# Optimization experiments

Hardware: AMD Instinct MI355X
Metric: run time of the kernel (lower is better)

Reference implementation:

```python
import jax, jax.numpy as jnp
import numpy as np

T, B = 128, 256      # seq_len, batch
D = 1024             # input_dim (embedding dim)
H = 1024             # hidden_dim
NQ = 8               # n_qubits
V = 32000            # vocab_size
TAGS = 1024          # tagset_size


def setup_inputs() -> dict:
    key = jax.random.key(0)
    ks = jax.random.split(key, 10)
    s = 0.05
    return {
        "sentence": jax.random.randint(ks[0], (T, B), 0, V),
        "emb": jax.random.normal(ks[1], (V, D), jnp.float32) * s,
        # gate order: forget, input, update, output (stacked on leading axis)
        "Wg": jax.random.normal(ks[2], (4, D + H, NQ), jnp.float32) * s,
        "bg": jax.random.normal(ks[3], (4, NQ), jnp.float32) * s,
        "theta": jax.random.normal(ks[4], (4, NQ), jnp.float32) * s,  # trainable RX angles
        "Wp": jax.random.normal(ks[5], (4, NQ, H), jnp.float32) * s,
        "bp": jax.random.normal(ks[6], (4, H), jnp.float32) * s,
        "W_tag": jax.random.normal(ks[7], (H, TAGS), jnp.float32) * s,
        "b_tag": jax.random.normal(ks[8], (TAGS,), jnp.float32) * s,
    }


def reference(sentence, emb, Wg, bg, theta, Wp, bp, W_tag, b_tag):
    embeds = emb[sentence]                      # (T, B, D)
    bsz = embeds.shape[1]
    hidden = Wp.shape[2]

    def step(carry, x):
        hx, cx = carry
        comb = jnp.concatenate([x, hx], axis=1)                       # (B, D+H)
        raw = jnp.einsum('bc,gcq->gbq', comb, Wg) + bg[:, None, :]    # (4, B, NQ)
        # QLayer: RX(x) then trainable RX(theta) per wire on |0>, measure Z
        # -> product state, <Z_i> = cos(raw_i + theta_i)  (exact)
        q = jnp.cos(raw + theta[:, None, :])                          # (4, B, NQ)
        proj = jnp.einsum('gbq,gqh->gbh', q, Wp) + bp[:, None, :]     # (4, B, H)
        f = jax.nn.sigmoid(proj[0])
        i = jax.nn.sigmoid(proj[1])
        g = jnp.tanh(proj[2])
        o = jax.nn.sigmoid(proj[3])
        cx = f * cx + i * g
        hx = o * jnp.tanh(cx)
        return (hx, cx), hx

    hx0 = jnp.zeros((bsz, hidden), embeds.dtype)
    cx0 = jnp.zeros((bsz, hidden), embeds.dtype)
    _, lstm_out = jax.lax.scan(step, (hx0, cx0), embeds)              # (T, B, H)
    tag_logits = lstm_out @ W_tag + b_tag                             # (T, B, TAGS)
    # torch applies log_softmax over dim=1 (the batch axis) -- faithful
    return jax.nn.log_softmax(tag_logits, axis=1)
```

## Files before the change

### kernel.cpp

```cpp
#include <hip/hip_runtime.h>
#include <hip/hip_bf16.h>
#include <stdint.h>

#define T_LEN 128
#define B_SZ  256
#define D_IN  1024
#define H_DIM 1024
#define NQ    8
#define VOCAB 32000
#define TAGS  1024

typedef __attribute__((ext_vector_type(8))) short short8;
typedef __attribute__((ext_vector_type(4))) float f32x4;

__device__ __forceinline__ unsigned short f2bf_bits(float x) {
    __hip_bfloat16 h = __float2bfloat16(x);
    unsigned short u; __builtin_memcpy(&u, &h, 2); return u;
}
__device__ __forceinline__ uint32_t pack_bf2(float a, float b) {
    return (uint32_t)f2bf_bits(a) | ((uint32_t)f2bf_bits(b) << 16);
}
__device__ __forceinline__ float2 unpack_bf2(uint32_t u) {
    float2 r;
    r.x = __uint_as_float(u << 16);
    r.y = __uint_as_float(u & 0xffff0000u);
    return r;
}
__device__ __forceinline__ float sigmoid_f(float x) {
    return 1.f / (1.f + __expf(-x));
}
__device__ __forceinline__ float tanh_f(float x) {
    return 1.f - 2.f / (__expf(2.f * x) + 1.f);
}
__device__ __forceinline__ void gload_lds16(void* lds_base, const void* gptr) {
    __builtin_amdgcn_global_load_lds(
        (__attribute__((address_space(1))) const void*)gptr,
        (__attribute__((address_space(3))) void*)lds_base,
        16, 0, 0);
}

__global__ __launch_bounds__(256) void k_wt_transpose(const float* __restrict__ W,
                                                      __hip_bfloat16* __restrict__ WtT) {
    __shared__ float tile[32][33];
    const int kb = blockIdx.x * 32, nb = blockIdx.y * 32;
    const int r = threadIdx.x >> 5, c = threadIdx.x & 31;
#pragma unroll
    for (int i = 0; i < 4; ++i)
        tile[r + 8 * i][c] = W[(size_t)(kb + r + 8 * i) * TAGS + nb + c];
    __syncthreads();
#pragma unroll
    for (int i = 0; i < 4; ++i)
        WtT[(size_t)(nb + r + 8 * i) * H_DIM + kb + c] = __float2bfloat16(tile[c][r + 8 * i]);
}

__global__ __launch_bounds__(1024) void k_qlstm(
    const int* __restrict__ sent, const float* __restrict__ emb,
    const float* __restrict__ Wg, const float* __restrict__ bg,
    const float* __restrict__ theta, const float* __restrict__ Wp,
    const float* __restrict__ bp, __hip_bfloat16* __restrict__ hb)
{
    __shared__ float comb[2048];
    __shared__ float red[32 * 17];
    __shared__ float qs[32];

    const int tid  = threadIdx.x;
    const int b    = blockIdx.x;
    const int o    = tid & 31;
    const int s    = tid >> 5;
    const int g    = o >> 3, q = o & 7;
    const int lane = tid & 63, wv = tid >> 6;

    uint32_t wg2[32];
#pragma unroll
    for (int j = 0; j < 32; ++j) {
        const int c0 = s * 64 + 2 * j;
        float a = Wg[((size_t)g * 2048 + c0) * 8 + q];
        float bb = Wg[((size_t)g * 2048 + c0 + 1) * 8 + q];
        wg2[j] = pack_bf2(a, bb);
    }
    uint32_t wp2[16];
#pragma unroll
    for (int j = 0; j < 16; ++j) {
        const int gg = j >> 2, jj = j & 3;
        float a = Wp[(size_t)(gg * 8 + 2 * jj) * H_DIM + tid];
        float bb = Wp[(size_t)(gg * 8 + 2 * jj + 1) * H_DIM + tid];
        wp2[j] = pack_bf2(a, bb);
    }
    float bpv[4];
#pragma unroll
    for (int gg = 0; gg < 4; ++gg) bpv[gg] = bp[gg * H_DIM + tid];
    const float bgt = (tid < 32) ? (bg[tid] + theta[tid]) : 0.f;

    float cx = 0.f;
    comb[1024 + tid] = 0.f;
    {
        const int w0 = sent[b];
        comb[tid] = emb[(size_t)w0 * D_IN + tid];
    }
    __syncthreads();

    for (int t = 0; t < T_LEN; ++t) {
        const int tn = (t + 1 < T_LEN) ? (t + 1) : (T_LEN - 1);
        const int wn = sent[tn * B_SZ + b];
        const float xnext = emb[(size_t)wn * D_IN + tid];

        float acc = 0.f;
        const float4* c4 = (const float4*)comb;
#pragma unroll
        for (int i = 0; i < 16; ++i) {
            float4 v = c4[s * 16 + i];
            float2 wa = unpack_bf2(wg2[2 * i]);
            float2 wb = unpack_bf2(wg2[2 * i + 1]);
            acc = fmaf(wa.x, v.x, acc);
            acc = fmaf(wa.y, v.y, acc);
            acc = fmaf(wb.x, v.z, acc);
            acc = fmaf(wb.y, v.w, acc);
        }
        acc += __shfl_xor(acc, 32, 64);
        if (lane < 32) red[lane * 17 + wv] = acc;
        __syncthreads();

        if (tid < 32) {
            float r = bgt;
#pragma unroll
            for (int w = 0; w < 16; ++w) r += red[tid * 17 + w];
            qs[tid] = __cosf(r);
        }
        comb[tid] = xnext;
        __syncthreads();

        const float4* q4 = (const float4*)qs;
        float pj[4];
#pragma unroll
        for (int gg = 0; gg < 4; ++gg) {
            float4 u = q4[2 * gg], v = q4[2 * gg + 1];
            float2 w0 = unpack_bf2(wp2[gg * 4 + 0]);
            float2 w1 = unpack_bf2(wp2[gg * 4 + 1]);
            float2 w2 = unpack_bf2(wp2[gg * 4 + 2]);
            float2 w3 = unpack_bf2(wp2[gg * 4 + 3]);
            pj[gg] = bpv[gg]
                   + u.x * w0.x + u.y * w0.y + u.z * w1.x + u.w * w1.y
                   + v.x * w2.x + v.y * w2.y + v.z * w3.x + v.w * w3.y;
        }
        const float f_ = sigmoid_f(pj[0]);
        const float i_ = sigmoid_f(pj[1]);
        const float g_ = tanh_f(pj[2]);
        const float o_ = sigmoid_f(pj[3]);
        cx = f_ * cx + i_ * g_;
        const float hv = o_ * tanh_f(cx);
        comb[1024 + tid] = hv;
        hb[((size_t)t * B_SZ + b) * H_DIM + tid] = __float2bfloat16(hv);
        __syncthreads();
    }
}

__global__ __launch_bounds__(256) void k_tag_gemm(const __hip_bfloat16* __restrict__ Hb,
                                                  const __hip_bfloat16* __restrict__ WtT,
                                                  float* __restrict__ out)
{
    __shared__ short As[128 * 32];
    __shared__ short Bs[128 * 32];
    const int m0 = blockIdx.x * 128, n0 = blockIdx.y * 128;
    const int tid = threadIdx.x, lane = tid & 63, wid = tid >> 6;
    const int wm = (wid & 1) * 64, wn = (wid >> 1) * 64;
    const int mrow = lane & 15, quad = lane >> 4;

    const short* Hs = (const short*)Hb;
    const short* Ws = (const short*)WtT;

    f32x4 acc[4][4];
#pragma unroll
    for (int mi = 0; mi < 4; ++mi)
#pragma unroll
        for (int ni = 0; ni < 4; ++ni)
            acc[mi][ni] = (f32x4){0.f, 0.f, 0.f, 0.f};

    for (int kt = 0; kt < 32; ++kt) {
        const int k0 = kt * 32;
        __syncthreads();
#pragma unroll
        for (int ch = 0; ch < 2; ++ch) {
            const int chunk = wid + ch * 4;
            const int row = chunk * 16 + (lane >> 2);
            const int kc = (lane & 3) * 8;
            gload_lds16(&As[chunk * 512], &Hs[(size_t)(m0 + row) * H_DIM + k0 + kc]);
            gload_lds16(&Bs[chunk * 512], &Ws[(size_t)(n0 + row) * H_DIM + k0 + kc]);
        }
        __syncthreads();

        short8 afr[4], bfr[4];
#pragma unroll
        for (int mi = 0; mi < 4; ++mi)
            afr[mi] = *(const short8*)&As[(wm + mi * 16 + mrow) * 32 + quad * 8];
#pragma unroll
        for (int ni = 0; ni < 4; ++ni)
            bfr[ni] = *(const short8*)&Bs[(wn + ni * 16 + mrow) * 32 + quad * 8];
#pragma unroll
        for (int mi = 0; mi < 4; ++mi)
#pragma unroll
            for (int ni = 0; ni < 4; ++ni)
                acc[mi][ni] = __builtin_amdgcn_mfma_f32_16x16x32_bf16(
                    afr[mi], bfr[ni], acc[mi][ni], 0, 0, 0);
    }

#pragma unroll
    for (int mi = 0; mi < 4; ++mi)
#pragma unroll
        for (int ni = 0; ni < 4; ++ni)
#pragma unroll
            for (int r = 0; r < 4; ++r) {
                const int grow = m0 + wm + mi * 16 + quad * 4 + r;
                const int gcol = n0 + wn + ni * 16 + mrow;
                out[(size_t)grow * TAGS + gcol] = acc[mi][ni][r];
            }
}

__global__ __launch_bounds__(256) void k_logsoftmax(float* __restrict__ out) {
    const int t = blockIdx.x;
    const int n = blockIdx.y * 256 + threadIdx.x;
    float* base = out + (size_t)t * B_SZ * TAGS + n;
    float m = -1e30f;
    for (int b = 0; b < B_SZ; ++b) m = fmaxf(m, base[(size_t)b * TAGS]);
    float s = 0.f;
    for (int b = 0; b < B_SZ; ++b) s += __expf(base[(size_t)b * TAGS] - m);
    const float lse = m + __logf(s);
    for (int b = 0; b < B_SZ; ++b) base[(size_t)b * TAGS] -= lse;
}

extern "C" void kernel_launch(void* const* d_in, const int* in_sizes, int n_in,
                              void* d_out, int out_size, void* d_ws, size_t ws_size,
                              hipStream_t stream) {
    (void)in_sizes; (void)n_in; (void)out_size; (void)ws_size;
    const int*   sent  = (const int*)d_in[0];
    const float* emb   = (const float*)d_in[1];
    const float* Wg    = (const float*)d_in[2];
    const float* bg    = (const float*)d_in[3];
    const float* theta = (const float*)d_in[4];
    const float* Wp    = (const float*)d_in[5];
    const float* bp    = (const float*)d_in[6];
    const float* Wt    = (const float*)d_in[7];
    float* out = (float*)d_out;

    __hip_bfloat16* hb  = (__hip_bfloat16*)d_ws;
    __hip_bfloat16* WtT = (__hip_bfloat16*)((char*)d_ws + (size_t)64 * 1024 * 1024);

    k_wt_transpose<<<dim3(32, 32), 256, 0, stream>>>(Wt, WtT);
    k_qlstm<<<dim3(B_SZ), 1024, 0, stream>>>(sent, emb, Wg, bg, theta, Wp, bp, hb);
    k_tag_gemm<<<dim3(256, 8), 256, 0, stream>>>(hb, WtT, out);
    k_logsoftmax<<<dim3(T_LEN, 4), 256, 0, stream>>>(out);
}
```

Before: 697.6 us.

## Remove a barrier per LSTM step, use packed FMA, online logsoftmax

In the recurrent kernel, every wave now redundantly reduces the 16 partial gate sums and computes the cosines into its own per-wave qs buffer. This removes one block-wide barrier per timestep. Gate weights are kept as fp32 pairs and accumulated with packed two-wide FMAs instead of bf16 unpacking, and the sentence indices are preloaded into LDS. The logsoftmax kernel uses a single-pass online max/sum with float2 accesses over half as many blocks. The trade-off is more redundant LDS reads and register pressure in exchange for fewer synchronisations and passes over the output.

```diff
diff --git a/kernel.cpp b/kernel.cpp
--- a/kernel.cpp
+++ b/kernel.cpp
@@ -12,6 +12,7 @@
 
 typedef __attribute__((ext_vector_type(8))) short short8;
 typedef __attribute__((ext_vector_type(4))) float f32x4;
+typedef __attribute__((ext_vector_type(2))) float v2f;
 
 __device__ __forceinline__ unsigned short f2bf_bits(float x) {
     __hip_bfloat16 h = __float2bfloat16(x);
@@ -25,6 +26,13 @@
     r.x = __uint_as_float(u << 16);
     r.y = __uint_as_float(u & 0xffff0000u);
     return r;
+}
+__device__ __forceinline__ v2f v2fma(v2f a, v2f b, v2f c) {
+#if __has_builtin(__builtin_elementwise_fma)
+    return __builtin_elementwise_fma(a, b, c);
+#else
+    c.x = fmaf(a.x, b.x, c.x); c.y = fmaf(a.y, b.y, c.y); return c;
+#endif
 }
 __device__ __forceinline__ float sigmoid_f(float x) {
     return 1.f / (1.f + __expf(-x));
@@ -61,7 +69,8 @@
 {
     __shared__ float comb[2048];
     __shared__ float red[32 * 17];
-    __shared__ float qs[32];
+    __shared__ float qs_w[16 * 32];
+    __shared__ int   sw[T_LEN];
 
     const int tid  = threadIdx.x;
     const int b    = blockIdx.x;
@@ -70,13 +79,12 @@
     const int g    = o >> 3, q = o & 7;
     const int lane = tid & 63, wv = tid >> 6;
 
-    uint32_t wg2[32];
+    v2f wgv[32];
 #pragma unroll
     for (int j = 0; j < 32; ++j) {
         const int c0 = s * 64 + 2 * j;
-        float a = Wg[((size_t)g * 2048 + c0) * 8 + q];
-        float bb = Wg[((size_t)g * 2048 + c0 + 1) * 8 + q];
-        wg2[j] = pack_bf2(a, bb);
+        wgv[j].x = Wg[((size_t)g * 2048 + c0) * 8 + q];
+        wgv[j].y = Wg[((size_t)g * 2048 + c0 + 1) * 8 + q];
     }
     uint32_t wp2[16];
 #pragma unroll
@@ -89,47 +97,46 @@
     float bpv[4];
 #pragma unroll
     for (int gg = 0; gg < 4; ++gg) bpv[gg] = bp[gg * H_DIM + tid];
-    const float bgt = (tid < 32) ? (bg[tid] + theta[tid]) : 0.f;
+    const float bgt = bg[o] + theta[o];
 
     float cx = 0.f;
     comb[1024 + tid] = 0.f;
-    {
-        const int w0 = sent[b];
-        comb[tid] = emb[(size_t)w0 * D_IN + tid];
-    }
+    if (tid < T_LEN) sw[tid] = sent[tid * B_SZ + b];
+    __syncthreads();
+    comb[tid] = emb[(size_t)sw[0] * D_IN + tid];
     __syncthreads();
 
     for (int t = 0; t < T_LEN; ++t) {
         const int tn = (t + 1 < T_LEN) ? (t + 1) : (T_LEN - 1);
-        const int wn = sent[tn * B_SZ + b];
-        const float xnext = emb[(size_t)wn * D_IN + tid];
-
-        float acc = 0.f;
+        const float xnext = emb[(size_t)sw[tn] * D_IN + tid];
+
+        v2f a0 = (v2f){0.f, 0.f}, a1 = (v2f){0.f, 0.f};
         const float4* c4 = (const float4*)comb;
 #pragma unroll
         for (int i = 0; i < 16; ++i) {
             float4 v = c4[s * 16 + i];
-            float2 wa = unpack_bf2(wg2[2 * i]);
-            float2 wb = unpack_bf2(wg2[2 * i + 1]);
-            acc = fmaf(wa.x, v.x, acc);
-            acc = fmaf(wa.y, v.y, acc);
-            acc = fmaf(wb.x, v.z, acc);
-            acc = fmaf(wb.y, v.w, acc);
-        }
+            a0 = v2fma(wgv[2 * i],     (v2f){v.x, v.y}, a0);
+            a1 = v2fma(wgv[2 * i + 1], (v2f){v.z, v.w}, a1);
+        }
+        float acc = (a0.x + a1.x) + (a0.y + a1.y);
         acc += __shfl_xor(acc, 32, 64);
-        if (lane < 32) red[lane * 17 + wv] = acc;
-        __syncthreads();
-
-        if (tid < 32) {
-            float r = bgt;
-#pragma unroll
-            for (int w = 0; w < 16; ++w) r += red[tid * 17 + w];
-            qs[tid] = __cosf(r);
-        }
+        if (lane < 32) red[o * 17 + wv] = acc;
+        __syncthreads();
+
         comb[tid] = xnext;
-        __syncthreads();
-
-        const float4* q4 = (const float4*)qs;
+
+        float r0 = 0.f, r1 = 0.f, r2 = 0.f, r3 = 0.f;
+#pragma unroll
+        for (int w = 0; w < 4; ++w) {
+            r0 += red[o * 17 + 4 * w + 0];
+            r1 += red[o * 17 + 4 * w + 1];
+            r2 += red[o * 17 + 4 * w + 2];
+            r3 += red[o * 17 + 4 * w + 3];
+        }
+        const float qv = __cosf(((r0 + r1) + (r2 + r3)) + bgt);
+        if (lane < 32) qs_w[wv * 32 + lane] = qv;
+
+        const float4* q4 = (const float4*)&qs_w[wv * 32];
         float pj[4];
 #pragma unroll
         for (int gg = 0; gg < 4; ++gg) {
@@ -217,14 +224,22 @@
 
 __global__ __launch_bounds__(256) void k_logsoftmax(float* __restrict__ out) {
     const int t = blockIdx.x;
-    const int n = blockIdx.y * 256 + threadIdx.x;
-    float* base = out + (size_t)t * B_SZ * TAGS + n;
-    float m = -1e30f;
-    for (int b = 0; b < B_SZ; ++b) m = fmaxf(m, base[(size_t)b * TAGS]);
-    float s = 0.f;
-    for (int b = 0; b < B_SZ; ++b) s += __expf(base[(size_t)b * TAGS] - m);
-    const float lse = m + __logf(s);
-    for (int b = 0; b < B_SZ; ++b) base[(size_t)b * TAGS] -= lse;
+    const int n2 = (blockIdx.y * 256 + threadIdx.x) * 2;
+    float* base = out + (size_t)t * B_SZ * TAGS + n2;
+    float mx = -1e30f, my = -1e30f, sx = 0.f, sy = 0.f;
+    for (int b = 0; b < B_SZ; ++b) {
+        float2 x = *(const float2*)&base[(size_t)b * TAGS];
+        float nmx = fmaxf(mx, x.x), nmy = fmaxf(my, x.y);
+        sx = sx * __expf(mx - nmx) + __expf(x.x - nmx);
+        sy = sy * __expf(my - nmy) + __expf(x.y - nmy);
+        mx = nmx; my = nmy;
+    }
+    const float lx = mx + __logf(sx), ly = my + __logf(sy);
+    for (int b = 0; b < B_SZ; ++b) {
+        float2 x = *(const float2*)&base[(size_t)b * TAGS];
+        x.x -= lx; x.y -= ly;
+        *(float2*)&base[(size_t)b * TAGS] = x;
+    }
 }
 
 extern "C" void kernel_launch(void* const* d_in, const int* in_sizes, int n_in,
@@ -247,5 +262,5 @@
     k_wt_transpose<<<dim3(32, 32), 256, 0, stream>>>(Wt, WtT);
     k_qlstm<<<dim3(B_SZ), 1024, 0, stream>>>(sent, emb, Wg, bg, theta, Wp, bp, hb);
     k_tag_gemm<<<dim3(256, 8), 256, 0, stream>>>(hb, WtT, out);
-    k_logsoftmax<<<dim3(T_LEN, 4), 256, 0, stream>>>(out);
-}
+    k_logsoftmax<<<dim3(T_LEN, 2), 256, 0, stream>>>(out);
+}
```

Result: slower. 732.4 us (+5.0%).
